# Kernel tuning notes

Measured on AMD Instinct MI355X. Metric: run time of the kernel, lower is better.

Reference implementation:

```python
import math
import jax, jax.numpy as jnp
import numpy as np

NUM_HEADS = 12
EPS = 1e-4


def softmax_kernel_features(data, proj, is_query):
    # data: [B,H,N,d], proj: [m,d] -> features [B,H,N,m]
    d = data.shape[-1]
    data_normalizer = 1.0 / math.sqrt(math.sqrt(d))
    ratio = 1.0 / math.sqrt(proj.shape[0])
    data_dash = jnp.einsum('bhnd,md->bhnm', data_normalizer * data, proj)
    diag_data = (jnp.sum(jnp.square(data), axis=-1, keepdims=True)
                 * 0.5 * data_normalizer * data_normalizer)  # [B,H,N,1]
    if is_query:
        stab = jnp.max(data_dash, axis=-1, keepdims=True)
    else:
        stab = jnp.max(data_dash)
    return ratio * (jnp.exp(data_dash - diag_data - stab) + EPS)


def setup_inputs() -> dict:
    key = jax.random.key(0)
    k0, k1, k2, k3, k4 = jax.random.split(key, 5)
    B, N, C, H = 8, 4096, 768, NUM_HEADS
    hd = C // H
    m = int(hd * math.log(hd))  # 266
    x = jax.random.normal(k0, (B, N, C), dtype=jnp.float32)
    W_qkv = jax.random.normal(k1, (C, 3 * C), dtype=jnp.float32) / math.sqrt(C)
    W_proj = jax.random.normal(k2, (C, C), dtype=jnp.float32) / math.sqrt(C)
    b_proj = jnp.zeros((C,), dtype=jnp.float32)
    proj_mat = jax.random.normal(k3, (m, hd), dtype=jnp.float32)
    return {'x': x, 'W_qkv': W_qkv, 'W_proj': W_proj, 'b_proj': b_proj,
            'proj_mat': proj_mat}


def reference(x, W_qkv, W_proj, b_proj, proj_mat):
    B, N, C = x.shape
    H = NUM_HEADS
    hd = C // H
    qkv = (x @ W_qkv).reshape(B, N, 3, H, hd)
    qkv = jnp.transpose(qkv, (2, 0, 3, 1, 4))  # [3,B,H,N,hd]
    q, k, v = qkv[0], qkv[1], qkv[2]
    q1 = softmax_kernel_features(q, proj_mat, is_query=True)   # [B,H,N,m]
    k1 = softmax_kernel_features(k, proj_mat, is_query=False)  # [B,H,N,m]
    # FAVOR+ non-causal linear attention
    kv = jnp.einsum('bhnm,bhnd->bhmd', k1, v)        # [B,H,m,hd]
    ksum = jnp.sum(k1, axis=2)                        # [B,H,m]
    z = 1.0 / jnp.einsum('bhnm,bhm->bhn', q1, ksum)  # [B,H,N]
    out = jnp.einsum('bhnm,bhmd->bhnd', q1, kv) * z[..., None]
    out = jnp.transpose(out, (0, 2, 1, 3)).reshape(B, N, C)
    return out @ W_proj + b_proj
```

## Files before the change

kernel.cpp:

```cpp
#include <hip/hip_runtime.h>
#include <hip/hip_bf16.h>
#include <math.h>

#define B_ 8
#define N_TOK 4096
#define C_ 768
#define H_ 12
#define HD_ 64
#define M_ 266
#define TC_ 2304
#define BH_ 96
#define ROWS_ 32768

#define M2 288
#define MP 296
#define KVS 72
#define K1S 40

#define DN 0.35355339059327373f
#define RATIO 0.06131393394849658f
#define FEPS 1e-4f
#define NEG_INF -3.0e38f

typedef __attribute__((ext_vector_type(4))) float f32x4;
typedef __attribute__((ext_vector_type(8))) short bf16x8;

__device__ __forceinline__ float bf2f(unsigned short u) {
  return __uint_as_float(((unsigned int)u) << 16);
}
__device__ __forceinline__ unsigned short f2bf(float f) {
  unsigned int x = __float_as_uint(f);
  unsigned int r = (x + 0x7fffu + ((x >> 16) & 1u)) >> 16;
  return (unsigned short)r;
}

#define GLOAD_LDS16(g, l) \
  __builtin_amdgcn_global_load_lds( \
      (const __attribute__((address_space(1))) void*)(g), \
      (__attribute__((address_space(3))) void*)(l), 16, 0, 0)

__global__ __launch_bounds__(256) void cast_bf16(
    const float* __restrict__ src, unsigned short* __restrict__ dst, int n)
{
  int i = (blockIdx.x * 256 + threadIdx.x) * 4;
  if (i < n) {
    float4 v = *(const float4*)&src[i];
    ushort4 u;
    u.x = f2bf(v.x); u.y = f2bf(v.y); u.z = f2bf(v.z); u.w = f2bf(v.w);
    *(ushort4*)&dst[i] = u;
  }
}

__global__ __launch_bounds__(256) void cast_pbf(
    const float* __restrict__ P, unsigned short* __restrict__ Pbf)
{
  int idx = blockIdx.x * 256 + threadIdx.x;
  if (idx < M2 * 64) {
    int m = idx >> 6;
    Pbf[idx] = (m < M_) ? f2bf(P[idx]) : (unsigned short)0;
  }
}

__global__ __launch_bounds__(256) void transpose_cast(
    const float* __restrict__ src, unsigned short* __restrict__ dst,
    int R, int Ccols)
{
  __shared__ float t[32][33];
  const int c0 = blockIdx.x * 32, r0 = blockIdx.y * 32;
  const int tx = threadIdx.x & 31, ty = threadIdx.x >> 5;
#pragma unroll
  for (int i = 0; i < 32; i += 8)
    t[ty + i][tx] = src[(size_t)(r0 + ty + i) * Ccols + c0 + tx];
  __syncthreads();
#pragma unroll
  for (int i = 0; i < 32; i += 8)
    dst[(size_t)(c0 + ty + i) * R + r0 + tx] = f2bf(t[tx][ty + i]);
}

template <int NT, int C_BF16, int HAS_BIAS>
__global__ __launch_bounds__(512) void gemm_pipe(
    const unsigned short* __restrict__ A, const unsigned short* __restrict__ Bt,
    const float* __restrict__ bias, void* __restrict__ Cptr)
{
  __shared__ unsigned short lds_[65536];
  const int Kdim = 768, Ndim = NT * 256;
  const int tid = threadIdx.x;
  const int lane = tid & 63, w = tid >> 6;

  const int id = blockIdx.x;
  const int nwg8 = (128 * NT) >> 3;
  const int sid = (id & 7) * nwg8 + (id >> 3);
  const int row0 = (sid / NT) * 256;
  const int col0 = (sid % NT) * 256;

  const int srow = tid >> 3;
  const int skb = (((tid & 7) ^ (srow & 7)) << 4);
  const size_t ag0 = (size_t)(row0 + srow) * Kdim + (skb >> 1);
  const size_t ag1 = (size_t)(row0 + 64 + srow) * Kdim + (skb >> 1);
  const size_t ag2 = (size_t)(row0 + 128 + srow) * Kdim + (skb >> 1);
  const size_t ag3 = (size_t)(row0 + 192 + srow) * Kdim + (skb >> 1);
  const size_t bg0 = (size_t)(col0 + srow) * Kdim + (skb >> 1);
  const size_t bg1 = (size_t)(col0 + 64 + srow) * Kdim + (skb >> 1);
  const size_t bg2 = (size_t)(col0 + 128 + srow) * Kdim + (skb >> 1);
  const size_t bg3 = (size_t)(col0 + 192 + srow) * Kdim + (skb >> 1);
  const int dst = tid * 8;

#define STAGE_Q(tt) do { \
    unsigned short* Lq_ = lds_ + ((tt) & 1) * 32768; \
    const int kq_ = (tt) * 64; \
    GLOAD_LDS16(A + ag0 + kq_, Lq_ + 0 * 4096 + dst); \
    GLOAD_LDS16(A + ag1 + kq_, Lq_ + 1 * 4096 + dst); \
    GLOAD_LDS16(A + ag2 + kq_, Lq_ + 2 * 4096 + dst); \
    GLOAD_LDS16(A + ag3 + kq_, Lq_ + 3 * 4096 + dst); \
    GLOAD_LDS16(Bt + bg0 + kq_, Lq_ + 16384 + 0 * 4096 + dst); \
    GLOAD_LDS16(Bt + bg1 + kq_, Lq_ + 16384 + 1 * 4096 + dst); \
    GLOAD_LDS16(Bt + bg2 + kq_, Lq_ + 16384 + 2 * 4096 + dst); \
    GLOAD_LDS16(Bt + bg3 + kq_, Lq_ + 16384 + 3 * 4096 + dst); \
  } while (0)

  const int fr = lane & 15, q = lane >> 4;
  const int wm = w >> 2, wn = w & 3;
  const int f7 = fr & 7;
  const int sl0 = ((q + 0) ^ f7) << 3;
  const int sl1 = ((q + 4) ^ f7) << 3;
  const int abase = (wm * 128 + fr) * 64;
  const int bbase = 16384 + (wn * 64 + fr) * 64;

  f32x4 acc[8][4];
  const f32x4 fz = {0.f, 0.f, 0.f, 0.f};
#pragma unroll
  for (int m = 0; m < 8; ++m)
#pragma unroll
    for (int n = 0; n < 4; ++n) acc[m][n] = fz;

  STAGE_Q(0);

#pragma unroll 1
  for (int t = 0; t < 12; ++t) {
    asm volatile("s_waitcnt vmcnt(0)" ::: "memory");
    __builtin_amdgcn_sched_barrier(0);
    __builtin_amdgcn_s_barrier();
    __builtin_amdgcn_sched_barrier(0);

    const unsigned short* Lb = lds_ + (t & 1) * 32768;
    bf16x8 av[8][2], bv[4][2];
#pragma unroll
    for (int m = 0; m < 8; ++m) {
      av[m][0] = *(const bf16x8*)&Lb[abase + m * 1024 + sl0];
      av[m][1] = *(const bf16x8*)&Lb[abase + m * 1024 + sl1];
    }
#pragma unroll
    for (int n = 0; n < 4; ++n) {
      bv[n][0] = *(const bf16x8*)&Lb[bbase + n * 1024 + sl0];
      bv[n][1] = *(const bf16x8*)&Lb[bbase + n * 1024 + sl1];
    }
    if (t < 11) STAGE_Q(t + 1);
    __builtin_amdgcn_s_setprio(1);
#pragma unroll
    for (int ks = 0; ks < 2; ++ks)
#pragma unroll
      for (int m = 0; m < 8; ++m)
#pragma unroll
        for (int n = 0; n < 4; ++n)
          acc[m][n] = __builtin_amdgcn_mfma_f32_16x16x32_bf16(av[m][ks], bv[n][ks], acc[m][n], 0, 0, 0);
    __builtin_amdgcn_s_setprio(0);
  }
#undef STAGE_Q

  const int orow = q * 4;
#pragma unroll
  for (int m = 0; m < 8; ++m) {
#pragma unroll
    for (int n = 0; n < 4; ++n) {
      const int c = col0 + wn * 64 + n * 16 + fr;
      float badd = 0.f;
      if constexpr (HAS_BIAS) badd = bias[c];
#pragma unroll
      for (int j = 0; j < 4; ++j) {
        const int r = row0 + wm * 128 + m * 16 + orow + j;
        float v = acc[m][n][j] + badd;
        if constexpr (C_BF16)
          ((unsigned short*)Cptr)[(size_t)r * Ndim + c] = f2bf(v);
        else
          ((float*)Cptr)[(size_t)r * Ndim + c] = v;
      }
    }
  }
}

__global__ __launch_bounds__(256) void kmax_reduce(
    const float* __restrict__ bmax, float* __restrict__ kmaxp, int n)
{
  __shared__ float red[4];
  float v = NEG_INF;
  for (int i = threadIdx.x; i < n; i += 256) v = fmaxf(v, bmax[i]);
#pragma unroll
  for (int off = 32; off >= 1; off >>= 1) v = fmaxf(v, __shfl_xor(v, off));
  if ((threadIdx.x & 63) == 0) red[threadIdx.x >> 6] = v;
  __syncthreads();
  if (threadIdx.x == 0)
    kmaxp[0] = DN * fmaxf(fmaxf(red[0], red[1]), fmaxf(red[2], red[3]));
}

__global__ __launch_bounds__(256) void kv_partial_mfma(
    const unsigned short* __restrict__ qkv, const unsigned short* __restrict__ Pbf,
    float* __restrict__ kvpart, float* __restrict__ ksumpart,
    float* __restrict__ bmax, float* __restrict__ Wpart)
{
  __shared__ unsigned short K_lds[64 * KVS];
  __shared__ unsigned short Vt_lds[64 * KVS];
  __shared__ unsigned short k1_lds[272 * K1S];
  __shared__ float diag_lds[64];
  const int tid = threadIdx.x;
  const int w = tid >> 6, lane = tid & 63;
  const int lr = lane & 15, q = lane >> 4;
  const int bh = blockIdx.x, chunk = blockIdx.y, z = blockIdx.z;
  const int b = bh / H_, h = bh % H_;
  const int ms = z * 8 + 2 * w;
  const int mc = (z == 1 && w == 3) ? 3 : 2;
  const int sn = 16 * w + (lane >> 2);
  const int sd0 = (lane & 3) * 16;
  const int vswz = sn ^ ((lane & 3) << 4);
  const int kswz = (lr >> 3) << 4;
  const f32x4 fz = {0.f, 0.f, 0.f, 0.f};

  f32x4 kvacc[3][4];
  float ksacc[3];
#pragma unroll
  for (int i = 0; i < 3; ++i) {
    ksacc[i] = 0.f;
#pragma unroll
    for (int dt = 0; dt < 4; ++dt) kvacc[i][dt] = fz;
  }
  float mx = NEG_INF;
  float vsum[16];
#pragma unroll
  for (int j = 0; j < 16; ++j) vsum[j] = 0.f;

  bf16x8 pf0[3], pf1[3];
#pragma unroll
  for (int i = 0; i < 3; ++i) {
    const unsigned short* prow = Pbf + (size_t)((ms + i) * 16 + lr) * 64 + q * 8;
    pf0[i] = *(const bf16x8*)prow;
    pf1[i] = *(const bf16x8*)(prow + 32);
  }

  const unsigned short* kbase = qkv + (size_t)(b * N_TOK + chunk * 512 + sn) * TC_ + C_ + h * HD_ + sd0;
  const size_t gstep = (size_t)64 * TC_;

  auto write_buf = [&](int4 wka, int4 wkb, int4 wva, int4 wvb) {
    *(int4*)&K_lds[sn * KVS + sd0] = wka;
    *(int4*)&K_lds[sn * KVS + sd0 + 8] = wkb;
    float sq = 0.f;
    const unsigned short* pk0 = (const unsigned short*)&wka;
#pragma unroll
    for (int j = 0; j < 8; ++j) { float f = bf2f(pk0[j]); sq = fmaf(f, f, sq); }
    const unsigned short* pk1 = (const unsigned short*)&wkb;
#pragma unroll
    for (int j = 0; j < 8; ++j) { float f = bf2f(pk1[j]); sq = fmaf(f, f, sq); }
    sq += __shfl_xor(sq, 1);
    sq += __shfl_xor(sq, 2);
    if ((lane & 3) == 0) diag_lds[sn] = 0.0625f * sq;
    const unsigned short* pv0 = (const unsigned short*)&wva;
    const unsigned short* pv1 = (const unsigned short*)&wvb;
#pragma unroll
    for (int j = 0; j < 8; ++j) {
      float vf = bf2f(pv0[j]);
      vsum[j] += vf;
      Vt_lds[(sd0 + j) * KVS + vswz] = pv0[j];
    }
#pragma unroll
    for (int j = 0; j < 8; ++j) {
      float vf = bf2f(pv1[j]);
      vsum[8 + j] += vf;
      Vt_lds[(sd0 + 8 + j) * KVS + vswz] = pv1[j];
    }
  };

  int4 ka = *(const int4*)kbase;
  int4 kb = *(const int4*)(kbase + 8);
  int4 va = *(const int4*)(kbase + C_);
  int4 vb = *(const int4*)(kbase + C_ + 8);
  write_buf(ka, kb, va, vb);
  asm volatile("s_waitcnt lgkmcnt(0)" ::: "memory");
  __builtin_amdgcn_s_barrier();

#pragma unroll 1
  for (int g = 0; g < 8; ++g) {
    if (g < 7) {
      const unsigned short* kr = kbase + (size_t)(g + 1) * gstep;
      ka = *(const int4*)kr;
      kb = *(const int4*)(kr + 8);
      va = *(const int4*)(kr + C_);
      vb = *(const int4*)(kr + C_ + 8);
    }
    __builtin_amdgcn_sched_barrier(0);

#pragma unroll
    for (int ks = 0; ks < 2; ++ks) {
      bf16x8 bkl[2][2];
#pragma unroll
      for (int t = 0; t < 2; ++t) {
        const int nrow = ((2 * ks + t) * 16 + lr) * KVS;
        bkl[t][0] = *(const bf16x8*)&K_lds[nrow + q * 8];
        bkl[t][1] = *(const bf16x8*)&K_lds[nrow + 32 + q * 8];
      }
      bf16x8 bv[4];
#pragma unroll
      for (int dt = 0; dt < 4; ++dt)
        bv[dt] = *(const bf16x8*)&Vt_lds[(dt * 16 + lr) * KVS + ((ks * 32 + q * 8) ^ (dt << 4))];

#pragma unroll
      for (int i = 0; i < 3; ++i) {
        if (i >= mc) continue;
        const int mt = ms + i;
        const int m = mt * 16 + lr;
        const int mrow = (mt * 16 + lr) * K1S;
        float loc = 0.f;
#pragma unroll
        for (int t = 0; t < 2; ++t) {
          f32x4 s = fz;
          s = __builtin_amdgcn_mfma_f32_16x16x32_bf16(bkl[t][0], pf0[i], s, 0, 0, 0);
          s = __builtin_amdgcn_mfma_f32_16x16x32_bf16(bkl[t][1], pf1[i], s, 0, 0, 0);
          if (m < M_)
            mx = fmaxf(mx, fmaxf(fmaxf(s[0], s[1]), fmaxf(s[2], s[3])));
          ushort4 uo;
          unsigned short* puo = (unsigned short*)&uo;
#pragma unroll
          for (int j = 0; j < 4; ++j) {
            const int nl = (2 * ks + t) * 16 + q * 4 + j;
            float k1f = 0.f;
            if (m < M_) {
              float dash = DN * s[j];
              k1f = __expf(dash - diag_lds[nl]);
            }
            loc += k1f;
            puo[j] = f2bf(k1f);
          }
          *(ushort4*)&k1_lds[mrow + ((t * 16 + q * 4) ^ kswz)] = uo;
        }
        ksacc[i] += loc;
        bf16x8 a1 = *(const bf16x8*)&k1_lds[mrow + ((q * 8) ^ kswz)];
#pragma unroll
        for (int dt = 0; dt < 4; ++dt)
          kvacc[i][dt] = __builtin_amdgcn_mfma_f32_16x16x32_bf16(a1, bv[dt], kvacc[i][dt], 0, 0, 0);
      }
    }

    if (g < 7) {
      __builtin_amdgcn_sched_barrier(0);
      __builtin_amdgcn_s_barrier();
      __builtin_amdgcn_sched_barrier(0);
      write_buf(ka, kb, va, vb);
      asm volatile("s_waitcnt lgkmcnt(0)" ::: "memory");
      __builtin_amdgcn_sched_barrier(0);
      __builtin_amdgcn_s_barrier();
      __builtin_amdgcn_sched_barrier(0);
    }
  }

  const size_t cb = (size_t)(chunk * BH_ + bh) * 64;
#pragma unroll
  for (int i = 0; i < 3; ++i) {
    if (i >= mc) continue;
    const int mt = ms + i;
#pragma unroll
    for (int dt = 0; dt < 4; ++dt) {
      float4 v4;
      v4.x = kvacc[i][dt][0]; v4.y = kvacc[i][dt][1];
      v4.z = kvacc[i][dt][2]; v4.w = kvacc[i][dt][3];
      *(float4*)&kvpart[(cb + dt * 16 + lr) * M2 + mt * 16 + q * 4] = v4;
    }
    float s = ksacc[i];
    s += __shfl_xor(s, 16);
    s += __shfl_xor(s, 32);
    if (lane < 16)
      ksumpart[(size_t)(chunk * BH_ + bh) * M2 + mt * 16 + lane] = s;
  }

#pragma unroll
  for (int off = 32; off >= 1; off >>= 1) mx = fmaxf(mx, __shfl_xor(mx, off));
#pragma unroll
  for (int j = 0; j < 16; ++j) {
    vsum[j] += __shfl_xor(vsum[j], 4);
    vsum[j] += __shfl_xor(vsum[j], 8);
    vsum[j] += __shfl_xor(vsum[j], 16);
    vsum[j] += __shfl_xor(vsum[j], 32);
  }
  __syncthreads();
  float* red = (float*)diag_lds;
  float* Wred = (float*)k1_lds;
  if (lane == 0) red[w] = mx;
  if (lane < 4) {
#pragma unroll
    for (int j = 0; j < 16; ++j)
      Wred[w * 64 + lane * 16 + j] = vsum[j];
  }
  __syncthreads();
  if (tid == 0)
    bmax[(z * 8 + chunk) * BH_ + bh] = fmaxf(fmaxf(red[0], red[1]), fmaxf(red[2], red[3]));
  if (z == 0 && tid < 64)
    Wpart[(size_t)(chunk * BH_ + bh) * 64 + tid] =
        Wred[tid] + Wred[64 + tid] + Wred[128 + tid] + Wred[192 + tid];
}

__global__ __launch_bounds__(256) void kv_reduce2(
    const float* __restrict__ kvpart, const float* __restrict__ ksumpart,
    const float* __restrict__ Wpart, const float* __restrict__ kmaxp,
    unsigned short* __restrict__ kvt_g, float* __restrict__ ksum_g)
{
  const int KVN = BH_ * 64 * M2;
  const int KSN = BH_ * M2;
  const float es = __expf(-kmaxp[0]);
  int idx = blockIdx.x * 256 + threadIdx.x;
  if (idx < KVN) {
    int m = idx % M2;
    float s = 0.f;
    if (m < M_) {
      float U = 0.f;
#pragma unroll
      for (int c = 0; c < 8; ++c) U += kvpart[(size_t)c * KVN + idx];
      const int d = (idx / M2) & 63;
      const int bh = idx / (M2 * 64);
      float Wsum = 0.f;
#pragma unroll
      for (int c = 0; c < 8; ++c) Wsum += Wpart[(size_t)(c * BH_ + bh) * 64 + d];
      s = RATIO * (es * U + FEPS * Wsum);
    }
    kvt_g[idx] = f2bf(s);
  } else if (idx < KVN + KSN) {
    int j = idx - KVN;
    int m = j % M2;
    float s = 0.f;
    if (m < M_) {
      float u = 0.f;
#pragma unroll
      for (int c = 0; c < 8; ++c) u += ksumpart[(size_t)c * KSN + j];
      s = RATIO * (es * u + FEPS * (float)N_TOK);
    }
    ksum_g[j] = s;
  }
}

__global__ __launch_bounds__(256) void attn_mfma(
    const unsigned short* __restrict__ qkv, const unsigned short* __restrict__ Pbf,
    const unsigned short* __restrict__ kvt_g, const float* __restrict__ ksum_g,
    unsigned short* __restrict__ attn)
{
  __shared__ unsigned short q1_lds[64 * MP];
  __shared__ unsigned short kvt_lds[64 * MP];
  __shared__ float ksum_lds[M2];
  __shared__ float z_lds[64];
  const int tid = threadIdx.x;
  const int bh = blockIdx.x;
  const int b = bh / H_, h = bh % H_;
  const int w = tid >> 6, lane = tid & 63;
  const int lr = lane & 15, q = lane >> 4;
  const f32x4 fz = {0.f, 0.f, 0.f, 0.f};

  {
    const unsigned short* src = kvt_g + (size_t)bh * 64 * M2;
#pragma unroll
    for (int i = 0; i < 9; ++i) {
      int chunk = i * 256 + tid;
      int r = chunk / 36, c = (chunk % 36) * 8;
      *(int4*)&kvt_lds[r * MP + c] = *(const int4*)(src + r * M2 + c);
    }
    if (tid < 72)
      *(float4*)&ksum_lds[tid * 4] = *(const float4*)(ksum_g + (size_t)bh * M2 + tid * 4);
    if (tid < 64) {
      const int4 z4 = {0, 0, 0, 0};
      *(int4*)&q1_lds[tid * MP + 272] = z4;
      *(int4*)&q1_lds[tid * MP + 280] = z4;
    }
  }
  __syncthreads();

#pragma unroll 1
  for (int gq = 0; gq < 4; ++gq) {
    const int n0 = (blockIdx.y * 4 + gq) * 64;

    const unsigned short* qrow = qkv + (size_t)(b * N_TOK + n0 + w * 16 + lr) * TC_ + h * HD_;
    bf16x8 bq0 = *(const bf16x8*)(qrow + q * 8);
    bf16x8 bq1 = *(const bf16x8*)(qrow + q * 8 + 32);
    float sq = 0.f;
    {
      const unsigned short* p0 = (const unsigned short*)&bq0;
      const unsigned short* p1 = (const unsigned short*)&bq1;
#pragma unroll
      for (int j = 0; j < 8; ++j) { float f = bf2f(p0[j]); sq = fmaf(f, f, sq); }
#pragma unroll
      for (int j = 0; j < 8; ++j) { float f = bf2f(p1[j]); sq = fmaf(f, f, sq); }
    }
    sq += __shfl_xor(sq, 16);
    sq += __shfl_xor(sq, 32);
    const float diag = 0.0625f * sq;

    f32x4 sacc[17];
#pragma unroll
    for (int mt = 0; mt < 17; ++mt) sacc[mt] = fz;
#pragma unroll
    for (int mt = 0; mt < 17; ++mt) {
      const unsigned short* prow = Pbf + (size_t)(mt * 16 + lr) * 64;
      bf16x8 ap0 = *(const bf16x8*)(prow + q * 8);
      bf16x8 ap1 = *(const bf16x8*)(prow + q * 8 + 32);
      sacc[mt] = __builtin_amdgcn_mfma_f32_16x16x32_bf16(ap0, bq0, sacc[mt], 0, 0, 0);
      sacc[mt] = __builtin_amdgcn_mfma_f32_16x16x32_bf16(ap1, bq1, sacc[mt], 0, 0, 0);
    }

    float mxr = NEG_INF;
#pragma unroll
    for (int mt = 0; mt < 17; ++mt) {
#pragma unroll
      for (int j = 0; j < 4; ++j) {
        int m = mt * 16 + q * 4 + j;
        if (m < M_) mxr = fmaxf(mxr, sacc[mt][j]);
      }
    }
    mxr = fmaxf(mxr, __shfl_xor(mxr, 16));
    mxr = fmaxf(mxr, __shfl_xor(mxr, 32));
    const float mxd = DN * mxr;

    float zp = 0.f;
#pragma unroll
    for (int mt = 0; mt < 17; ++mt) {
      ushort4 uo;
      unsigned short* puo = (unsigned short*)&uo;
#pragma unroll
      for (int j = 0; j < 4; ++j) {
        const int m = mt * 16 + q * 4 + j;
        float q1f = 0.f;
        if (m < M_) {
          float dash = DN * sacc[mt][j];
          q1f = RATIO * (__expf(dash - diag - mxd) + FEPS);
        }
        zp = fmaf(q1f, ksum_lds[m], zp);
        puo[j] = f2bf(q1f);
      }
      *(ushort4*)&q1_lds[(w * 16 + lr) * MP + mt * 16 + q * 4] = uo;
    }
    zp += __shfl_xor(zp, 16);
    zp += __shfl_xor(zp, 32);
    if (q == 0) z_lds[w * 16 + lr] = 1.0f / zp;

    f32x4 oacc[4];
#pragma unroll
    for (int dt = 0; dt < 4; ++dt) oacc[dt] = fz;
#pragma unroll
    for (int ks = 0; ks < 9; ++ks) {
      bf16x8 aq = *(const bf16x8*)&q1_lds[(w * 16 + lr) * MP + ks * 32 + q * 8];
#pragma unroll
      for (int dt = 0; dt < 4; ++dt) {
        bf16x8 bkv = *(const bf16x8*)&kvt_lds[(dt * 16 + lr) * MP + ks * 32 + q * 8];
        oacc[dt] = __builtin_amdgcn_mfma_f32_16x16x32_bf16(aq, bkv, oacc[dt], 0, 0, 0);
      }
    }

    float zz[4];
#pragma unroll
    for (int j = 0; j < 4; ++j) zz[j] = z_lds[w * 16 + q * 4 + j];
#pragma unroll
    for (int dt = 0; dt < 4; ++dt) {
#pragma unroll
      for (int j = 0; j < 4; ++j) {
        const int r = b * N_TOK + n0 + w * 16 + q * 4 + j;
        attn[(size_t)r * C_ + h * HD_ + dt * 16 + lr] = f2bf(oacc[dt][j] * zz[j]);
      }
    }
  }
}

extern "C" void kernel_launch(void* const* d_in, const int* in_sizes, int n_in,
                              void* d_out, int out_size, void* d_ws, size_t ws_size,
                              hipStream_t stream) {
  const float* x     = (const float*)d_in[0];
  const float* Wqkv  = (const float*)d_in[1];
  const float* Wproj = (const float*)d_in[2];
  const float* bproj = (const float*)d_in[3];
  const float* P     = (const float*)d_in[4];
  float* out = (float*)d_out;
  float* ws = (float*)d_ws;

  unsigned short* qkv    = (unsigned short*)ws;
  unsigned short* xb     = (unsigned short*)(ws + 37748736);
  float*          kvpart = ws + 37748736;
  unsigned short* attn   = (unsigned short*)(ws + 37748736);
  float* ksumpart = ws + 51904512;
  unsigned short* kvt_g  = (unsigned short*)(ws + 52125696);
  float* ksum_g   = ws + 53010432;
  float* bmax     = ws + 53038080;
  float* kmaxp    = ws + 53041152;
  unsigned short* Pbf    = (unsigned short*)(ws + 53041216);
  unsigned short* Wqkvt  = (unsigned short*)(ws + 53050432);
  unsigned short* Wprojt = (unsigned short*)(ws + 53935168);
  float* Wpart    = ws + 54230080;

  cast_bf16<<<dim3(24576), 256, 0, stream>>>(x, xb, ROWS_ * C_);
  transpose_cast<<<dim3(72, 24), 256, 0, stream>>>(Wqkv, Wqkvt, C_, TC_);
  transpose_cast<<<dim3(24, 24), 256, 0, stream>>>(Wproj, Wprojt, C_, C_);
  cast_pbf<<<dim3(72), 256, 0, stream>>>(P, Pbf);

  gemm_pipe<9, 1, 0><<<dim3(1152), 512, 0, stream>>>(xb, Wqkvt, nullptr, qkv);
  kv_partial_mfma<<<dim3(96, 8, 2), 256, 0, stream>>>(qkv, Pbf, kvpart, ksumpart, bmax, Wpart);
  kmax_reduce<<<dim3(1), 256, 0, stream>>>(bmax, kmaxp, 1536);
  kv_reduce2<<<dim3(7020), 256, 0, stream>>>(kvpart, ksumpart, Wpart, kmaxp, kvt_g, ksum_g);
  attn_mfma<<<dim3(96, 16), 256, 0, stream>>>(qkv, Pbf, kvt_g, ksum_g, attn);
  gemm_pipe<3, 0, 1><<<dim3(384), 512, 0, stream>>>(attn, Wprojt, bproj, out);
}
```

Before: 453.9 us.

## Merge kv_partial z-split into one 512-thread block sharing K/V staging

Replaces the two blocks per (bh, chunk) that each covered half of the m-tiles with one 512-thread block of 8 waves covering all m-tiles. The K/V tile is now loaded, staged into LDS and squared only once instead of twice, and each thread loads 8 elements instead of 16. The end-of-block reductions are reworked for 8 waves, and the bmax count passed to kmax_reduce is halved. In exchange the grid has half as many blocks, so there is less parallelism to hide latency, and the larger blocks may lower occupancy.

```diff
diff --git a/kernel.cpp b/kernel.cpp
--- a/kernel.cpp
+++ b/kernel.cpp
@@ -202,7 +202,7 @@
     kmaxp[0] = DN * fmaxf(fmaxf(red[0], red[1]), fmaxf(red[2], red[3]));
 }
 
-__global__ __launch_bounds__(256) void kv_partial_mfma(
+__global__ __launch_bounds__(512) void kv_partial_mfma(
     const unsigned short* __restrict__ qkv, const unsigned short* __restrict__ Pbf,
     float* __restrict__ kvpart, float* __restrict__ ksumpart,
     float* __restrict__ bmax, float* __restrict__ Wpart)
@@ -211,16 +211,17 @@
   __shared__ unsigned short Vt_lds[64 * KVS];
   __shared__ unsigned short k1_lds[272 * K1S];
   __shared__ float diag_lds[64];
+  __shared__ float red8[8];
   const int tid = threadIdx.x;
   const int w = tid >> 6, lane = tid & 63;
   const int lr = lane & 15, q = lane >> 4;
-  const int bh = blockIdx.x, chunk = blockIdx.y, z = blockIdx.z;
+  const int bh = blockIdx.x, chunk = blockIdx.y;
   const int b = bh / H_, h = bh % H_;
-  const int ms = z * 8 + 2 * w;
-  const int mc = (z == 1 && w == 3) ? 3 : 2;
-  const int sn = 16 * w + (lane >> 2);
-  const int sd0 = (lane & 3) * 16;
-  const int vswz = sn ^ ((lane & 3) << 4);
+  const int ms = 2 * w;
+  const int mc = (w == 7) ? 3 : 2;
+  const int sn = tid >> 3;
+  const int sd0 = (tid & 7) * 8;
+  const int vswz = sn ^ (((sd0 >> 4) & 3) << 4);
   const int kswz = (lr >> 3) << 4;
   const f32x4 fz = {0.f, 0.f, 0.f, 0.f};
 
@@ -233,9 +234,9 @@
     for (int dt = 0; dt < 4; ++dt) kvacc[i][dt] = fz;
   }
   float mx = NEG_INF;
-  float vsum[16];
-#pragma unroll
-  for (int j = 0; j < 16; ++j) vsum[j] = 0.f;
+  float vsum[8];
+#pragma unroll
+  for (int j = 0; j < 8; ++j) vsum[j] = 0.f;
 
   bf16x8 pf0[3], pf1[3];
 #pragma unroll
@@ -248,40 +249,28 @@
   const unsigned short* kbase = qkv + (size_t)(b * N_TOK + chunk * 512 + sn) * TC_ + C_ + h * HD_ + sd0;
   const size_t gstep = (size_t)64 * TC_;
 
-  auto write_buf = [&](int4 wka, int4 wkb, int4 wva, int4 wvb) {
-    *(int4*)&K_lds[sn * KVS + sd0] = wka;
-    *(int4*)&K_lds[sn * KVS + sd0 + 8] = wkb;
+  auto write_buf = [&](int4 wk, int4 wv) {
+    *(int4*)&K_lds[sn * KVS + sd0] = wk;
     float sq = 0.f;
-    const unsigned short* pk0 = (const unsigned short*)&wka;
-#pragma unroll
-    for (int j = 0; j < 8; ++j) { float f = bf2f(pk0[j]); sq = fmaf(f, f, sq); }
-    const unsigned short* pk1 = (const unsigned short*)&wkb;
-#pragma unroll
-    for (int j = 0; j < 8; ++j) { float f = bf2f(pk1[j]); sq = fmaf(f, f, sq); }
+    const unsigned short* pk = (const unsigned short*)&wk;
+#pragma unroll
+    for (int j = 0; j < 8; ++j) { float f = bf2f(pk[j]); sq = fmaf(f, f, sq); }
     sq += __shfl_xor(sq, 1);
     sq += __shfl_xor(sq, 2);
-    if ((lane & 3) == 0) diag_lds[sn] = 0.0625f * sq;
-    const unsigned short* pv0 = (const unsigned short*)&wva;
-    const unsigned short* pv1 = (const unsigned short*)&wvb;
+    sq += __shfl_xor(sq, 4);
+    if ((tid & 7) == 0) diag_lds[sn] = 0.0625f * sq;
+    const unsigned short* pv = (const unsigned short*)&wv;
 #pragma unroll
     for (int j = 0; j < 8; ++j) {
-      float vf = bf2f(pv0[j]);
+      float vf = bf2f(pv[j]);
       vsum[j] += vf;
-      Vt_lds[(sd0 + j) * KVS + vswz] = pv0[j];
-    }
-#pragma unroll
-    for (int j = 0; j < 8; ++j) {
-      float vf = bf2f(pv1[j]);
-      vsum[8 + j] += vf;
-      Vt_lds[(sd0 + 8 + j) * KVS + vswz] = pv1[j];
+      Vt_lds[(sd0 + j) * KVS + vswz] = pv[j];
     }
   };
 
   int4 ka = *(const int4*)kbase;
-  int4 kb = *(const int4*)(kbase + 8);
   int4 va = *(const int4*)(kbase + C_);
-  int4 vb = *(const int4*)(kbase + C_ + 8);
-  write_buf(ka, kb, va, vb);
+  write_buf(ka, va);
   asm volatile("s_waitcnt lgkmcnt(0)" ::: "memory");
   __builtin_amdgcn_s_barrier();
 
@@ -290,9 +279,7 @@
     if (g < 7) {
       const unsigned short* kr = kbase + (size_t)(g + 1) * gstep;
       ka = *(const int4*)kr;
-      kb = *(const int4*)(kr + 8);
       va = *(const int4*)(kr + C_);
-      vb = *(const int4*)(kr + C_ + 8);
     }
     __builtin_amdgcn_sched_barrier(0);
 
@@ -351,7 +338,7 @@
       __builtin_amdgcn_sched_barrier(0);
       __builtin_amdgcn_s_barrier();
       __builtin_amdgcn_sched_barrier(0);
-      write_buf(ka, kb, va, vb);
+      write_buf(ka, va);
       asm volatile("s_waitcnt lgkmcnt(0)" ::: "memory");
       __builtin_amdgcn_sched_barrier(0);
       __builtin_amdgcn_s_barrier();
@@ -381,27 +368,32 @@
 #pragma unroll
   for (int off = 32; off >= 1; off >>= 1) mx = fmaxf(mx, __shfl_xor(mx, off));
 #pragma unroll
-  for (int j = 0; j < 16; ++j) {
-    vsum[j] += __shfl_xor(vsum[j], 4);
+  for (int j = 0; j < 8; ++j) {
     vsum[j] += __shfl_xor(vsum[j], 8);
     vsum[j] += __shfl_xor(vsum[j], 16);
     vsum[j] += __shfl_xor(vsum[j], 32);
   }
+  if (lane == 0) red8[w] = mx;
   __syncthreads();
-  float* red = (float*)diag_lds;
   float* Wred = (float*)k1_lds;
-  if (lane == 0) red[w] = mx;
-  if (lane < 4) {
-#pragma unroll
-    for (int j = 0; j < 16; ++j)
-      Wred[w * 64 + lane * 16 + j] = vsum[j];
+  if (lane < 8) {
+#pragma unroll
+    for (int j = 0; j < 8; ++j)
+      Wred[w * 64 + lane * 8 + j] = vsum[j];
   }
   __syncthreads();
-  if (tid == 0)
-    bmax[(z * 8 + chunk) * BH_ + bh] = fmaxf(fmaxf(red[0], red[1]), fmaxf(red[2], red[3]));
-  if (z == 0 && tid < 64)
-    Wpart[(size_t)(chunk * BH_ + bh) * 64 + tid] =
-        Wred[tid] + Wred[64 + tid] + Wred[128 + tid] + Wred[192 + tid];
+  if (tid == 0) {
+    float m0 = red8[0];
+#pragma unroll
+    for (int ww = 1; ww < 8; ++ww) m0 = fmaxf(m0, red8[ww]);
+    bmax[chunk * BH_ + bh] = m0;
+  }
+  if (tid < 64) {
+    float s = 0.f;
+#pragma unroll
+    for (int ww = 0; ww < 8; ++ww) s += Wred[ww * 64 + tid];
+    Wpart[(size_t)(chunk * BH_ + bh) * 64 + tid] = s;
+  }
 }
 
 __global__ __launch_bounds__(256) void kv_reduce2(
@@ -601,8 +593,8 @@
   cast_pbf<<<dim3(72), 256, 0, stream>>>(P, Pbf);
 
   gemm_pipe<9, 1, 0><<<dim3(1152), 512, 0, stream>>>(xb, Wqkvt, nullptr, qkv);
-  kv_partial_mfma<<<dim3(96, 8, 2), 256, 0, stream>>>(qkv, Pbf, kvpart, ksumpart, bmax, Wpart);
-  kmax_reduce<<<dim3(1), 256, 0, stream>>>(bmax, kmaxp, 1536);
+  kv_partial_mfma<<<dim3(96, 8), 512, 0, stream>>>(qkv, Pbf, kvpart, ksumpart, bmax, Wpart);
+  kmax_reduce<<<dim3(1), 256, 0, stream>>>(bmax, kmaxp, 768);
   kv_reduce2<<<dim3(7020), 256, 0, stream>>>(kvpart, ksumpart, Wpart, kmaxp, kvt_g, ksum_g);
   attn_mfma<<<dim3(96, 16), 256, 0, stream>>>(qkv, Pbf, kvt_g, ksum_g, attn);
   gemm_pipe<3, 0, 1><<<dim3(384), 512, 0, stream>>>(attn, Wprojt, bproj, out);
```

Result: no change. 453.9 us (median of 2 runs) (+0.0%).
